# Optimization experiments

Hardware: AMD Instinct MI355X
Metric: run time of the kernel (lower is better)

Reference implementation:

```python
import jax, jax.numpy as jnp
import numpy as np

TEMP1 = 4.0  # local_temp1 default


def setup_inputs() -> dict:
    key = jax.random.key(0)
    k1, k2 = jax.random.split(key)
    query = jax.random.normal(k1, (256, 768, 96), dtype=jnp.float32)
    context = jax.random.normal(k2, (256, 768, 19, 19), dtype=jnp.float32)
    return {"query": query, "context": context}


def reference(query, context):
    # query: [B, ndf, Q]; context: [B, ndf, ih, iw]
    B, ndf, Q = query.shape
    ih, iw = context.shape[2], context.shape[3]
    S = ih * iw
    ctx = context.reshape(B, ndf, S)            # [B, ndf, S]
    # attn = contextT @ query -> [B, S, Q]
    attn = jnp.einsum('bds,bdq->bsq', ctx, query)
    # softmax over query dim
    attn = jax.nn.softmax(attn, axis=-1)
    # transpose to [B, Q, S], temperature scale, softmax over source dim
    attn = jnp.swapaxes(attn, 1, 2) * TEMP1
    attn = jax.nn.softmax(attn, axis=-1)        # [B, Q, S]
    # weightedContext = context @ attn^T -> [B, ndf, Q]
    weighted_context = jnp.einsum('bds,bqs->bdq', ctx, attn)
    attn_map = attn.reshape(B, Q, ih, iw)
    return weighted_context, attn_map
```

## Files before the change

### kernel.cpp

```cpp
#include <hip/hip_runtime.h>

#define NB 256
#define NDF 768
#define NQ 96
#define NS 361
#define LDT 40
#define LDP 392
#define WSROW 368
#define WS_LOG_BYTES ((size_t)NB * NQ * WSROW * 2)

typedef short bf16x8_t __attribute__((ext_vector_type(8)));
typedef float f32x2_t __attribute__((ext_vector_type(2)));
typedef float f32x4_t __attribute__((ext_vector_type(4)));
typedef float f32x4u_t __attribute__((ext_vector_type(4), aligned(4)));
typedef unsigned int u32x4_t __attribute__((ext_vector_type(4)));

__device__ __forceinline__ unsigned pack_hi(unsigned b_, unsigned a_) {
    return __builtin_amdgcn_perm(b_, a_, 0x07060302u);
}
__device__ __forceinline__ unsigned short f2bf(float x) {
    unsigned u = __float_as_uint(x);
    u += 0x7FFFu + ((u >> 16) & 1u);
    return (unsigned short)(u >> 16);
}
__device__ __forceinline__ float bf2f(unsigned short h) {
    return __uint_as_float(((unsigned)h) << 16);
}

__device__ __forceinline__ void cvt8(const float* x, bf16x8_t& hi, bf16x8_t& lo) {
    unsigned uh[8]; float fl[8];
#pragma unroll
    for (int j = 0; j < 8; ++j) {
        unsigned u = __float_as_uint(x[j]);
        uh[j] = u;
        fl[j] = x[j] - __uint_as_float(u & 0xFFFF0000u);
    }
    u32x4_t h, l;
    h[0] = pack_hi(uh[1], uh[0]); h[1] = pack_hi(uh[3], uh[2]);
    h[2] = pack_hi(uh[5], uh[4]); h[3] = pack_hi(uh[7], uh[6]);
    l[0] = pack_hi(__float_as_uint(fl[1]), __float_as_uint(fl[0]));
    l[1] = pack_hi(__float_as_uint(fl[3]), __float_as_uint(fl[2]));
    l[2] = pack_hi(__float_as_uint(fl[5]), __float_as_uint(fl[4]));
    l[3] = pack_hi(__float_as_uint(fl[7]), __float_as_uint(fl[6]));
    hi = __builtin_bit_cast(bf16x8_t, h);
    lo = __builtin_bit_cast(bf16x8_t, l);
}

__device__ __forceinline__ void block_sync_lds() {
    asm volatile("s_waitcnt lgkmcnt(0)" ::: "memory");
    __builtin_amdgcn_s_barrier();
    __builtin_amdgcn_sched_barrier(0);
}

#define GLD(D, A)       asm volatile("global_load_dword %0, %1, off" : "=v"(D) : "v"(A))
#define GLDO(D, A, O)   asm volatile("global_load_dword %0, %1, off offset:" #O : "=v"(D) : "v"(A))
#define GLD2(D, A)      asm volatile("global_load_dwordx2 %0, %1, off" : "=v"(D) : "v"(A))
#define GLD2O(D, A, O)  asm volatile("global_load_dwordx2 %0, %1, off offset:" #O : "=v"(D) : "v"(A))
#define VMWAIT(N) { asm volatile("s_waitcnt vmcnt(" #N ")"); __builtin_amdgcn_sched_barrier(0); }

template<int MODE>
__global__ __launch_bounds__(384, 3) void k1_gemm1_softmaxq(
    const float* __restrict__ Qg, const float* __restrict__ Cg,
    unsigned short* __restrict__ WsLog, float* __restrict__ AoutF)
{
    __shared__ __align__(16) unsigned short sQhi[2][NQ * LDT];
    __shared__ __align__(16) unsigned short sQlo[2][NQ * LDT];

    const int x = blockIdx.x;
    const int b = (x & 7) * 32 + (x >> 4);
    const int h = (x >> 3) & 1;

    const int tid = threadIdx.x;
    const int wv = tid >> 6;
    const int lane = tid & 63;
    const int ll = lane & 15;
    const int lg = lane >> 4;
    const int llh = (ll >> 3) & 1;
    const int s0 = 192 * h;
    const int qq = tid % 96;
    const int koct = tid / 96;
    const int spRaw = s0 + 32 * wv + 2 * ll;
    const int sp0c  = min(spRaw, NS - 2);
    const bool bsel = (spRaw > NS - 2);
    const int stoff = qq * LDT + 8 * (koct ^ ((qq >> 3) & 3));

    const float* __restrict__ qg = Qg + (size_t)b * NDF * NQ;
    const float* __restrict__ cg = Cg + (size_t)b * NDF * NS;
    const float* __restrict__ cgl = cg + sp0c;

    f32x4_t acc[6][2];
#pragma unroll
    for (int i = 0; i < 6; ++i)
#pragma unroll
        for (int j = 0; j < 2; ++j) acc[i][j] = (f32x4_t)0.0f;

    float qv0[8], qv1[8];
    f32x2_t rcA[8], rcB[8], rcC[8];

#define ISSUE_Q(K0, QV) { \
    unsigned long long qa = (unsigned long long)(qg + ((K0) + 8 * koct) * NQ + qq); \
    GLD (QV[0], qa);        GLDO(QV[1], qa, 384); \
    GLDO(QV[2], qa, 768);   GLDO(QV[3], qa, 1152); \
    GLDO(QV[4], qa, 1536);  GLDO(QV[5], qa, 1920); \
    GLDO(QV[6], qa, 2304);  GLDO(QV[7], qa, 2688); }

#define ISSUE_CTX(K0, R) { \
    unsigned long long p0 = (unsigned long long)(cgl + (size_t)((K0) + 8 * lg) * NS); \
    unsigned long long p1 = p0 + 3u * 1444u; \
    unsigned long long p2 = p0 + 6u * 1444u; \
    GLD2 (R[0], p0); GLD2O(R[1], p0, 1444); GLD2O(R[2], p0, 2888); \
    GLD2 (R[3], p1); GLD2O(R[4], p1, 1444); GLD2O(R[5], p1, 2888); \
    GLD2 (R[6], p2); GLD2O(R[7], p2, 1444); }

#define STAGEQ(QV, CUR) { \
    bf16x8_t qh, ql; \
    cvt8(QV, qh, ql); \
    *(bf16x8_t*)&sQhi[CUR][stoff] = qh; \
    *(bf16x8_t*)&sQlo[CUR][stoff] = ql; }

#define MFMAPH(R, CUR) { \
    float xe[8], xo[8]; \
    _Pragma("unroll") \
    for (int j = 0; j < 8; ++j) { \
        xe[j] = bsel ? R[j][1] : R[j][0]; \
        xo[j] = R[j][1]; } \
    bf16x8_t B0h, B0l, B1h, B1l; \
    cvt8(xe, B0h, B0l); \
    cvt8(xo, B1h, B1l); \
    _Pragma("unroll") \
    for (int mt = 0; mt < 6; ++mt) { \
        int ro = (16 * mt + ll) * LDT + 8 * (lg ^ ((2 * mt + llh) & 3)); \
        bf16x8_t Ah = *(const bf16x8_t*)&sQhi[CUR][ro]; \
        bf16x8_t Al = *(const bf16x8_t*)&sQlo[CUR][ro]; \
        acc[mt][0] = __builtin_amdgcn_mfma_f32_16x16x32_bf16(Ah, B0h, acc[mt][0], 0, 0, 0); \
        acc[mt][0] = __builtin_amdgcn_mfma_f32_16x16x32_bf16(Ah, B0l, acc[mt][0], 0, 0, 0); \
        acc[mt][0] = __builtin_amdgcn_mfma_f32_16x16x32_bf16(Al, B0h, acc[mt][0], 0, 0, 0); \
        acc[mt][1] = __builtin_amdgcn_mfma_f32_16x16x32_bf16(Ah, B1h, acc[mt][1], 0, 0, 0); \
        acc[mt][1] = __builtin_amdgcn_mfma_f32_16x16x32_bf16(Ah, B1l, acc[mt][1], 0, 0, 0); \
        acc[mt][1] = __builtin_amdgcn_mfma_f32_16x16x32_bf16(Al, B1h, acc[mt][1], 0, 0, 0); } }

#define ITER(C, USE, FILL, QISS, QSTG, CUR, NXT) { \
    ISSUE_Q(((C) + 2) * 32, QISS); \
    ISSUE_CTX(((C) + 2) * 32, FILL); \
    VMWAIT(32); \
    MFMAPH(USE, CUR); \
    VMWAIT(24); \
    STAGEQ(QSTG, NXT); \
    block_sync_lds(); }

    ISSUE_Q(0, qv0);   ISSUE_CTX(0, rcA);
    ISSUE_Q(32, qv1);  ISSUE_CTX(32, rcB);
    VMWAIT(24);
    STAGEQ(qv0, 0);
    block_sync_lds();

    for (int cc = 0; cc < 18; cc += 6) {
        ITER(cc + 0, rcA, rcC, qv0, qv1, 0, 1);
        ITER(cc + 1, rcB, rcA, qv1, qv0, 1, 0);
        ITER(cc + 2, rcC, rcB, qv0, qv1, 0, 1);
        ITER(cc + 3, rcA, rcC, qv1, qv0, 1, 0);
        ITER(cc + 4, rcB, rcA, qv0, qv1, 0, 1);
        ITER(cc + 5, rcC, rcB, qv1, qv0, 1, 0);
    }
    ITER(18, rcA, rcC, qv0, qv1, 0, 1);
    ITER(19, rcB, rcA, qv1, qv0, 1, 0);
    ITER(20, rcC, rcB, qv0, qv1, 0, 1);
    ITER(21, rcA, rcC, qv1, qv0, 1, 0);
    VMWAIT(16);
    MFMAPH(rcB, 0);
    VMWAIT(8);
    STAGEQ(qv1, 1);
    block_sync_lds();
    VMWAIT(0);
    MFMAPH(rcC, 1);

#undef ISSUE_Q
#undef ISSUE_CTX
#undef STAGEQ
#undef MFMAPH
#undef ITER

#pragma unroll
    for (int nt = 0; nt < 2; ++nt) {
        float m = -3.0e38f;
#pragma unroll
        for (int mt = 0; mt < 6; ++mt)
#pragma unroll
            for (int r = 0; r < 4; ++r) m = fmaxf(m, acc[mt][nt][r]);
        m = fmaxf(m, __shfl_xor(m, 16));
        m = fmaxf(m, __shfl_xor(m, 32));
        float sum = 0.0f;
#pragma unroll
        for (int mt = 0; mt < 6; ++mt)
#pragma unroll
            for (int r = 0; r < 4; ++r) {
                float e = __expf(acc[mt][nt][r] - m);
                acc[mt][nt][r] = e;
                sum += e;
            }
        sum += __shfl_xor(sum, 16);
        sum += __shfl_xor(sum, 32);
        float inv = 4.0f / sum;
#pragma unroll
        for (int mt = 0; mt < 6; ++mt)
#pragma unroll
            for (int r = 0; r < 4; ++r) acc[mt][nt][r] *= inv;
    }

    if constexpr (MODE >= 1) {
        unsigned short* wr = WsLog + (size_t)b * NQ * WSROW;
#pragma unroll
        for (int mt = 0; mt < 6; ++mt)
#pragma unroll
            for (int nt = 0; nt < 2; ++nt)
#pragma unroll
                for (int r = 0; r < 4; ++r) {
                    int q = 16 * mt + 4 * lg + r;
                    int s = s0 + 32 * wv + 2 * ll + nt;
                    if (s < NS) wr[q * WSROW + s] = f2bf(acc[mt][nt][r]);
                }
    } else {
        float* aout = AoutF + (size_t)b * NQ * NS;
#pragma unroll
        for (int mt = 0; mt < 6; ++mt)
#pragma unroll
            for (int nt = 0; nt < 2; ++nt)
#pragma unroll
                for (int r = 0; r < 4; ++r) {
                    int q = 16 * mt + 4 * lg + r;
                    int s = s0 + 32 * wv + 2 * ll + nt;
                    if (s < NS) aout[(size_t)q * NS + s] = acc[mt][nt][r];
                }
    }
}

__global__ __launch_bounds__(256) void k15_softmaxs(float* __restrict__ Aout)
{
    const int b = blockIdx.x;
    const int q = blockIdx.y * 4 + (threadIdx.x >> 6);
    const int lane = threadIdx.x & 63;
    float* __restrict__ row = Aout + ((size_t)b * NQ + q) * NS;
    const int c0 = 6 * lane;

    float v[6];
#pragma unroll
    for (int i = 0; i < 6; ++i) v[i] = (c0 + i < NS) ? row[c0 + i] : -INFINITY;
    float m = v[0];
#pragma unroll
    for (int i = 1; i < 6; ++i) m = fmaxf(m, v[i]);
#pragma unroll
    for (int o = 1; o < 64; o <<= 1) m = fmaxf(m, __shfl_xor(m, o));
    float e[6], sum = 0.0f;
#pragma unroll
    for (int i = 0; i < 6; ++i) { e[i] = __expf(v[i] - m); sum += e[i]; }
#pragma unroll
    for (int o = 1; o < 64; o <<= 1) sum += __shfl_xor(sum, o);
    float inv = 1.0f / sum;
#pragma unroll
    for (int i = 0; i < 6; ++i) if (c0 + i < NS) row[c0 + i] = e[i] * inv;
}

template<bool FUSED>
__global__ __launch_bounds__(512, 4) void k2_gemm2(
    const float* __restrict__ Cg, const unsigned short* __restrict__ WsLog,
    const float* __restrict__ AttnF, float* __restrict__ Wout, float* __restrict__ AoutF)
{
    extern __shared__ char smem2[];
    unsigned short* sP = (unsigned short*)smem2;
    unsigned* sPd = (unsigned*)smem2;
    float* sMax = (float*)(smem2 + NQ * LDP * 2);
    float* sInv = sMax + NQ;

    const int x = blockIdx.x;
    const int b = (x & 7) * 32 + (x >> 5);
    const int quarter = (x >> 3) & 3;
    const int tid = threadIdx.x;
    const int wv = tid >> 6;
    const int lane = tid & 63;
    const int ll = lane & 15;
    const int lg = lane >> 4;

    if constexpr (FUSED) {
        const unsigned* __restrict__ wsd = (const unsigned*)(WsLog + (size_t)b * NQ * WSROW);
        for (int i = tid; i < NQ * 184; i += 512) {
            int r = i / 184, c = i - r * 184;
            sPd[r * 196 + c] = wsd[i];
        }
        for (int i = tid; i < NQ * 12; i += 512) {
            int r = i / 12, c = i - r * 12;
            sPd[r * 196 + 184 + c] = 0;
        }
        __syncthreads();

        const int l32 = tid & 31;
        const int rbase = tid >> 5;
#pragma unroll
        for (int pass = 0; pass < 6; ++pass) {
            int row = pass * 16 + rbase;
            float m = -3.0e38f;
#pragma unroll
            for (int j = 0; j < 6; ++j) {
                int dw = l32 + 32 * j;
                if (dw < 184) {
                    unsigned u = sPd[row * 196 + dw];
                    float v0 = bf2f((unsigned short)(u & 0xFFFFu));
                    float v1 = bf2f((unsigned short)(u >> 16));
                    if (2 * dw < NS) m = fmaxf(m, v0);
                    if (2 * dw + 1 < NS) m = fmaxf(m, v1);
                }
            }
#pragma unroll
            for (int o = 1; o < 32; o <<= 1) m = fmaxf(m, __shfl_xor(m, o));
            if (l32 == 0) sMax[row] = m;
        }
        __syncthreads();
#pragma unroll
        for (int pass = 0; pass < 6; ++pass) {
            int row = pass * 16 + rbase;
            float m = sMax[row];
            float sum = 0.0f;
#pragma unroll
            for (int j = 0; j < 6; ++j) {
                int dw = l32 + 32 * j;
                if (dw < 184) {
                    unsigned u = sPd[row * 196 + dw];
                    float v0 = bf2f((unsigned short)(u & 0xFFFFu));
                    float v1 = bf2f((unsigned short)(u >> 16));
                    float e0 = (2 * dw < NS) ? __expf(v0 - m) : 0.0f;
                    float e1 = (2 * dw + 1 < NS) ? __expf(v1 - m) : 0.0f;
                    sum += e0 + e1;
                    sPd[row * 196 + dw] = ((unsigned)f2bf(e1) << 16) | (unsigned)f2bf(e0);
                }
            }
#pragma unroll
            for (int o = 1; o < 32; o <<= 1) sum += __shfl_xor(sum, o);
            if (l32 == 0) sInv[row] = sum;
        }
        __syncthreads();
        if (tid < NQ) sInv[tid] = 1.0f / sInv[tid];
        __syncthreads();
        if (quarter == 0) {
            float* aout = AoutF + (size_t)b * NQ * NS;
            for (int i = tid; i < NQ * NS; i += 512) {
                int q = i / NS, s = i - q * NS;
                aout[i] = bf2f(sP[q * LDP + s]) * sInv[q];
            }
        }
    } else {
        const float* __restrict__ attn = AttnF + (size_t)b * NQ * NS;
        for (int i = tid; i < NQ * 181; i += 512) {
            int row = i / 181, p = i - row * 181;
            float x0 = attn[row * NS + 2 * p];
            float x1 = (p < 180) ? attn[row * NS + 2 * p + 1] : 0.0f;
            sPd[row * 196 + p] = pack_hi(__float_as_uint(x1), __float_as_uint(x0));
        }
        for (int i = tid; i < NQ * 15; i += 512) {
            int row = i / 15, p = i - row * 15;
            sPd[row * 196 + 181 + p] = 0;
        }
        __syncthreads();
    }

    f32x4_t acc[3][3];
#pragma unroll
    for (int i = 0; i < 3; ++i)
#pragma unroll
        for (int j = 0; j < 3; ++j) acc[i][j] = (f32x4_t)0.0f;

    const int dw = wv >> 1, qw = wv & 1;
    const float* __restrict__ cq = Cg + (size_t)b * NDF * NS + (size_t)(quarter * 192) * NS;

#pragma unroll
    for (int c = 0; c < 12; ++c) {
        bf16x8_t Bf[3];
#pragma unroll
        for (int nt = 0; nt < 3; ++nt) {
            int row = 16 * (3 * qw + nt) + ll;
            Bf[nt] = *(const bf16x8_t*)&sP[row * LDP + 32 * c + 8 * lg];
        }
#pragma unroll
        for (int i = 0; i < 3; ++i) {
            int d = 16 * (3 * dw + i) + ll;
            const float* ap = cq + (size_t)d * NS + 32 * c + 8 * lg;
            u32x4_t u;
            if (c < 11) {
                f32x4u_t a0 = *(const f32x4u_t*)ap;
                f32x4u_t a1 = *(const f32x4u_t*)(ap + 4);
                u[0] = pack_hi(__float_as_uint(a0[1]), __float_as_uint(a0[0]));
                u[1] = pack_hi(__float_as_uint(a0[3]), __float_as_uint(a0[2]));
                u[2] = pack_hi(__float_as_uint(a1[1]), __float_as_uint(a1[0]));
                u[3] = pack_hi(__float_as_uint(a1[3]), __float_as_uint(a1[2]));
            } else {
                float t[8];
#pragma unroll
                for (int e = 0; e < 8; ++e) {
                    int s = 352 + 8 * lg + e;
                    t[e] = (s < NS) ? ap[e] : 0.0f;
                }
                u[0] = pack_hi(__float_as_uint(t[1]), __float_as_uint(t[0]));
                u[1] = pack_hi(__float_as_uint(t[3]), __float_as_uint(t[2]));
                u[2] = pack_hi(__float_as_uint(t[5]), __float_as_uint(t[4]));
                u[3] = pack_hi(__float_as_uint(t[7]), __float_as_uint(t[6]));
            }
            bf16x8_t Af = __builtin_bit_cast(bf16x8_t, u);
#pragma unroll
            for (int nt = 0; nt < 3; ++nt)
                acc[i][nt] = __builtin_amdgcn_mfma_f32_16x16x32_bf16(Af, Bf[nt], acc[i][nt], 0, 0, 0);
        }
    }

    float* wout = Wout + (size_t)b * NDF * NQ;
    float invq[3];
#pragma unroll
    for (int nt = 0; nt < 3; ++nt) {
        if constexpr (FUSED) invq[nt] = sInv[16 * (3 * qw + nt) + ll];
        else invq[nt] = 1.0f;
    }
#pragma unroll
    for (int i = 0; i < 3; ++i)
#pragma unroll
        for (int nt = 0; nt < 3; ++nt)
#pragma unroll
            for (int r = 0; r < 4; ++r) {
                int d = quarter * 192 + 16 * (3 * dw + i) + 4 * lg + r;
                int q = 16 * (3 * qw + nt) + ll;
                wout[(size_t)d * NQ + q] = acc[i][nt][r] * invq[nt];
            }
}

extern "C" void kernel_launch(void* const* d_in, const int* in_sizes, int n_in,
                              void* d_out, int out_size, void* d_ws, size_t ws_size,
                              hipStream_t stream) {
    const float* Qg = (const float*)d_in[0];
    const float* Cg = (const float*)d_in[1];
    float* Wout = (float*)d_out;
    float* Aout = Wout + (size_t)NB * NDF * NQ;

    const int smem2 = NQ * LDP * 2 + NQ * 8;

    if (ws_size >= WS_LOG_BYTES) {
        unsigned short* wsLog = (unsigned short*)d_ws;
        k1_gemm1_softmaxq<1><<<dim3(NB * 2), dim3(384), 0, stream>>>(Qg, Cg, wsLog, nullptr);
        (void)hipFuncSetAttribute((const void*)k2_gemm2<true>,
                                  hipFuncAttributeMaxDynamicSharedMemorySize, smem2);
        k2_gemm2<true><<<dim3(NB * 4), dim3(512), smem2, stream>>>(
            Cg, wsLog, nullptr, Wout, Aout);
    } else {
        k1_gemm1_softmaxq<0><<<dim3(NB * 2), dim3(384), 0, stream>>>(Qg, Cg, nullptr, Aout);
        k15_softmaxs<<<dim3(NB, 24), dim3(256), 0, stream>>>(Aout);
        (void)hipFuncSetAttribute((const void*)k2_gemm2<false>,
                                  hipFuncAttributeMaxDynamicSharedMemorySize, smem2);
        k2_gemm2<false><<<dim3(NB * 4), dim3(512), smem2, stream>>>(
            Cg, nullptr, Aout, Wout, Aout);
    }
}
```

Baseline: 212.0 us.

## Emit bf16 context copy from gemm1 and read it in gemm2

The first kernel now writes a bf16-truncated, padded copy of the context tensor to workspace while it streams the context for GEMM1. The second kernel reads those bf16 rows directly instead of reloading fp32 context and packing it, which roughly halves GEMM2's context traffic. The GEMM1 pipeline also moves from triple to double buffering of context registers with adjusted wait counts, which lowers register pressure. The cost is extra global stores in kernel 1 and a larger workspace requirement, with the old paths kept as fallbacks when the workspace is too small.

```diff
diff --git a/kernel.cpp b/kernel.cpp
--- a/kernel.cpp
+++ b/kernel.cpp
@@ -7,7 +7,10 @@
 #define LDT 40
 #define LDP 392
 #define WSROW 368
+#define CSROW 368
 #define WS_LOG_BYTES ((size_t)NB * NQ * WSROW * 2)
+#define WS_CTX_BYTES ((size_t)NB * NDF * CSROW * 2)
+#define WS_FULL_BYTES (WS_LOG_BYTES + WS_CTX_BYTES)
 
 typedef short bf16x8_t __attribute__((ext_vector_type(8)));
 typedef float f32x2_t __attribute__((ext_vector_type(2)));
@@ -56,12 +59,16 @@
 #define GLDO(D, A, O)   asm volatile("global_load_dword %0, %1, off offset:" #O : "=v"(D) : "v"(A))
 #define GLD2(D, A)      asm volatile("global_load_dwordx2 %0, %1, off" : "=v"(D) : "v"(A))
 #define GLD2O(D, A, O)  asm volatile("global_load_dwordx2 %0, %1, off offset:" #O : "=v"(D) : "v"(A))
-#define VMWAIT(N) { asm volatile("s_waitcnt vmcnt(" #N ")"); __builtin_amdgcn_sched_barrier(0); }
+#define GST(A, D)       asm volatile("global_store_dword %0, %1, off" :: "v"(A), "v"(D))
+#define GSTO(A, D, O)   asm volatile("global_store_dword %0, %1, off offset:" #O :: "v"(A), "v"(D))
+#define VMWAIT_(N) { asm volatile("s_waitcnt vmcnt(" #N ")"); __builtin_amdgcn_sched_barrier(0); }
+#define VMWAIT(N) VMWAIT_(N)
 
 template<int MODE>
 __global__ __launch_bounds__(384, 3) void k1_gemm1_softmaxq(
     const float* __restrict__ Qg, const float* __restrict__ Cg,
-    unsigned short* __restrict__ WsLog, float* __restrict__ AoutF)
+    unsigned short* __restrict__ WsLog, unsigned* __restrict__ WsCtxD,
+    float* __restrict__ AoutF)
 {
     __shared__ __align__(16) unsigned short sQhi[2][NQ * LDT];
     __shared__ __align__(16) unsigned short sQlo[2][NQ * LDT];
@@ -82,11 +89,14 @@
     const int spRaw = s0 + 32 * wv + 2 * ll;
     const int sp0c  = min(spRaw, NS - 2);
     const bool bsel = (spRaw > NS - 2);
+    const int pairIdx = 96 * h + 16 * wv + ll;
+    const bool wok = (MODE == 2) && (pairIdx <= 180);
     const int stoff = qq * LDT + 8 * (koct ^ ((qq >> 3) & 3));
 
     const float* __restrict__ qg = Qg + (size_t)b * NDF * NQ;
     const float* __restrict__ cg = Cg + (size_t)b * NDF * NS;
     const float* __restrict__ cgl = cg + sp0c;
+    unsigned* __restrict__ wsc = (MODE == 2) ? (WsCtxD + (size_t)b * NDF * 184 + pairIdx) : nullptr;
 
     f32x4_t acc[6][2];
 #pragma unroll
@@ -94,15 +104,15 @@
 #pragma unroll
         for (int j = 0; j < 2; ++j) acc[i][j] = (f32x4_t)0.0f;
 
-    float qv0[8], qv1[8];
-    f32x2_t rcA[8], rcB[8], rcC[8];
-
-#define ISSUE_Q(K0, QV) { \
+    float qv[8];
+    f32x2_t rcA[8], rcB[8];
+
+#define ISSUE_Q(K0) { \
     unsigned long long qa = (unsigned long long)(qg + ((K0) + 8 * koct) * NQ + qq); \
-    GLD (QV[0], qa);        GLDO(QV[1], qa, 384); \
-    GLDO(QV[2], qa, 768);   GLDO(QV[3], qa, 1152); \
-    GLDO(QV[4], qa, 1536);  GLDO(QV[5], qa, 1920); \
-    GLDO(QV[6], qa, 2304);  GLDO(QV[7], qa, 2688); }
+    GLD (qv[0], qa);        GLDO(qv[1], qa, 384); \
+    GLDO(qv[2], qa, 768);   GLDO(qv[3], qa, 1152); \
+    GLDO(qv[4], qa, 1536);  GLDO(qv[5], qa, 1920); \
+    GLDO(qv[6], qa, 2304);  GLDO(qv[7], qa, 2688); }
 
 #define ISSUE_CTX(K0, R) { \
     unsigned long long p0 = (unsigned long long)(cgl + (size_t)((K0) + 8 * lg) * NS); \
@@ -112,9 +122,24 @@
     GLD2 (R[3], p1); GLD2O(R[4], p1, 1444); GLD2O(R[5], p1, 2888); \
     GLD2 (R[6], p2); GLD2O(R[7], p2, 1444); }
 
-#define STAGEQ(QV, CUR) { \
+#define ISSUE_ST(K0, R) { \
+    if (wok) { \
+        unsigned st[8]; \
+        _Pragma("unroll") \
+        for (int j = 0; j < 8; ++j) { \
+            unsigned lo_ = bsel ? __float_as_uint(R[j][1]) : __float_as_uint(R[j][0]); \
+            unsigned hi_ = bsel ? 0u : __float_as_uint(R[j][1]); \
+            st[j] = pack_hi(hi_, lo_); \
+        } \
+        unsigned long long a0 = (unsigned long long)(wsc + (size_t)((K0) + 8 * lg) * 184); \
+        unsigned long long a1 = a0 + 4416u; \
+        GST (a0, st[0]); GSTO(a0, st[1], 736); GSTO(a0, st[2], 1472); \
+        GSTO(a0, st[3], 2208); GSTO(a0, st[4], 2944); GSTO(a0, st[5], 3680); \
+        GST (a1, st[6]); GSTO(a1, st[7], 736); } }
+
+#define STAGEQ(CUR) { \
     bf16x8_t qh, ql; \
-    cvt8(QV, qh, ql); \
+    cvt8(qv, qh, ql); \
     *(bf16x8_t*)&sQhi[CUR][stoff] = qh; \
     *(bf16x8_t*)&sQlo[CUR][stoff] = ql; }
 
@@ -139,43 +164,44 @@
         acc[mt][1] = __builtin_amdgcn_mfma_f32_16x16x32_bf16(Ah, B1l, acc[mt][1], 0, 0, 0); \
         acc[mt][1] = __builtin_amdgcn_mfma_f32_16x16x32_bf16(Al, B1h, acc[mt][1], 0, 0, 0); } }
 
-#define ITER(C, USE, FILL, QISS, QSTG, CUR, NXT) { \
-    ISSUE_Q(((C) + 2) * 32, QISS); \
-    ISSUE_CTX(((C) + 2) * 32, FILL); \
-    VMWAIT(32); \
+#define ITER(C, USE, FILL, CUR, NXT, W1, W2) { \
+    ISSUE_Q(((C) + 1) * 32); \
+    ISSUE_CTX(((C) + 1) * 32, FILL); \
+    VMWAIT(W1); \
+    ISSUE_ST((C) * 32, USE); \
     MFMAPH(USE, CUR); \
-    VMWAIT(24); \
-    STAGEQ(QSTG, NXT); \
+    VMWAIT(W2); \
+    STAGEQ(NXT); \
     block_sync_lds(); }
 
-    ISSUE_Q(0, qv0);   ISSUE_CTX(0, rcA);
-    ISSUE_Q(32, qv1);  ISSUE_CTX(32, rcB);
-    VMWAIT(24);
-    STAGEQ(qv0, 0);
+    ISSUE_Q(0);
+    ISSUE_CTX(0, rcA);
+    VMWAIT(8);
+    STAGEQ(0);
     block_sync_lds();
 
-    for (int cc = 0; cc < 18; cc += 6) {
-        ITER(cc + 0, rcA, rcC, qv0, qv1, 0, 1);
-        ITER(cc + 1, rcB, rcA, qv1, qv0, 1, 0);
-        ITER(cc + 2, rcC, rcB, qv0, qv1, 0, 1);
-        ITER(cc + 3, rcA, rcC, qv1, qv0, 1, 0);
-        ITER(cc + 4, rcB, rcA, qv0, qv1, 0, 1);
-        ITER(cc + 5, rcC, rcB, qv1, qv0, 1, 0);
-    }
-    ITER(18, rcA, rcC, qv0, qv1, 0, 1);
-    ITER(19, rcB, rcA, qv1, qv0, 1, 0);
-    ITER(20, rcC, rcB, qv0, qv1, 0, 1);
-    ITER(21, rcA, rcC, qv1, qv0, 1, 0);
-    VMWAIT(16);
-    MFMAPH(rcB, 0);
-    VMWAIT(8);
-    STAGEQ(qv1, 1);
-    block_sync_lds();
-    VMWAIT(0);
-    MFMAPH(rcC, 1);
+    if constexpr (MODE == 2) {
+        ITER(0, rcA, rcB, 0, 1, 16, 16);
+        for (int c = 1; c < 22; c += 2) {
+            ITER(c,     rcB, rcA, 1, 0, 24, 16);
+            ITER(c + 1, rcA, rcB, 0, 1, 24, 16);
+        }
+        VMWAIT(8);
+        ISSUE_ST(23 * 32, rcB);
+        MFMAPH(rcB, 1);
+    } else {
+        ITER(0, rcA, rcB, 0, 1, 16, 8);
+        for (int c = 1; c < 22; c += 2) {
+            ITER(c,     rcB, rcA, 1, 0, 16, 8);
+            ITER(c + 1, rcA, rcB, 0, 1, 16, 8);
+        }
+        VMWAIT(0);
+        MFMAPH(rcB, 1);
+    }
 
 #undef ISSUE_Q
 #undef ISSUE_CTX
+#undef ISSUE_ST
 #undef STAGEQ
 #undef MFMAPH
 #undef ITER
@@ -232,6 +258,7 @@
                     if (s < NS) aout[(size_t)q * NS + s] = acc[mt][nt][r];
                 }
     }
+    asm volatile("s_waitcnt vmcnt(0)" ::: "memory");
 }
 
 __global__ __launch_bounds__(256) void k15_softmaxs(float* __restrict__ Aout)
@@ -260,9 +287,10 @@
     for (int i = 0; i < 6; ++i) if (c0 + i < NS) row[c0 + i] = e[i] * inv;
 }
 
-template<bool FUSED>
+template<int MODE>
 __global__ __launch_bounds__(512, 4) void k2_gemm2(
     const float* __restrict__ Cg, const unsigned short* __restrict__ WsLog,
+    const unsigned short* __restrict__ WsCtx,
     const float* __restrict__ AttnF, float* __restrict__ Wout, float* __restrict__ AoutF)
 {
     extern __shared__ char smem2[];
@@ -280,7 +308,7 @@
     const int ll = lane & 15;
     const int lg = lane >> 4;
 
-    if constexpr (FUSED) {
+    if constexpr (MODE >= 1) {
         const unsigned* __restrict__ wsd = (const unsigned*)(WsLog + (size_t)b * NQ * WSROW);
         for (int i = tid; i < NQ * 184; i += 512) {
             int r = i / 184, c = i - r * 184;
@@ -369,6 +397,8 @@
 
     const int dw = wv >> 1, qw = wv & 1;
     const float* __restrict__ cq = Cg + (size_t)b * NDF * NS + (size_t)(quarter * 192) * NS;
+    const unsigned short* __restrict__ cb =
+        (MODE == 2) ? (WsCtx + ((size_t)b * NDF + quarter * 192) * CSROW) : nullptr;
 
 #pragma unroll
     for (int c = 0; c < 12; ++c) {
@@ -381,28 +411,37 @@
 #pragma unroll
         for (int i = 0; i < 3; ++i) {
             int d = 16 * (3 * dw + i) + ll;
-            const float* ap = cq + (size_t)d * NS + 32 * c + 8 * lg;
-            u32x4_t u;
-            if (c < 11) {
-                f32x4u_t a0 = *(const f32x4u_t*)ap;
-                f32x4u_t a1 = *(const f32x4u_t*)(ap + 4);
-                u[0] = pack_hi(__float_as_uint(a0[1]), __float_as_uint(a0[0]));
-                u[1] = pack_hi(__float_as_uint(a0[3]), __float_as_uint(a0[2]));
-                u[2] = pack_hi(__float_as_uint(a1[1]), __float_as_uint(a1[0]));
-                u[3] = pack_hi(__float_as_uint(a1[3]), __float_as_uint(a1[2]));
+            bf16x8_t Af;
+            if constexpr (MODE == 2) {
+                if (c < 11 || lg < 2) {
+                    Af = *(const bf16x8_t*)&cb[(size_t)d * CSROW + 32 * c + 8 * lg];
+                } else {
+                    Af = (bf16x8_t)0;
+                }
             } else {
-                float t[8];
-#pragma unroll
-                for (int e = 0; e < 8; ++e) {
-                    int s = 352 + 8 * lg + e;
-                    t[e] = (s < NS) ? ap[e] : 0.0f;
+                const float* ap = cq + (size_t)d * NS + 32 * c + 8 * lg;
+                u32x4_t u;
+                if (c < 11) {
+                    f32x4u_t a0 = *(const f32x4u_t*)ap;
+                    f32x4u_t a1 = *(const f32x4u_t*)(ap + 4);
+                    u[0] = pack_hi(__float_as_uint(a0[1]), __float_as_uint(a0[0]));
+                    u[1] = pack_hi(__float_as_uint(a0[3]), __float_as_uint(a0[2]));
+                    u[2] = pack_hi(__float_as_uint(a1[1]), __float_as_uint(a1[0]));
+                    u[3] = pack_hi(__float_as_uint(a1[3]), __float_as_uint(a1[2]));
+                } else {
+                    float t[8];
+#pragma unroll
+                    for (int e = 0; e < 8; ++e) {
+                        int s = 352 + 8 * lg + e;
+                        t[e] = (s < NS) ? ap[e] : 0.0f;
+                    }
+                    u[0] = pack_hi(__float_as_uint(t[1]), __float_as_uint(t[0]));
+                    u[1] = pack_hi(__float_as_uint(t[3]), __float_as_uint(t[2]));
+                    u[2] = pack_hi(__float_as_uint(t[5]), __float_as_uint(t[4]));
+                    u[3] = pack_hi(__float_as_uint(t[7]), __float_as_uint(t[6]));
                 }
-                u[0] = pack_hi(__float_as_uint(t[1]), __float_as_uint(t[0]));
-                u[1] = pack_hi(__float_as_uint(t[3]), __float_as_uint(t[2]));
-                u[2] = pack_hi(__float_as_uint(t[5]), __float_as_uint(t[4]));
-                u[3] = pack_hi(__float_as_uint(t[7]), __float_as_uint(t[6]));
+                Af = __builtin_bit_cast(bf16x8_t, u);
             }
-            bf16x8_t Af = __builtin_bit_cast(bf16x8_t, u);
 #pragma unroll
             for (int nt = 0; nt < 3; ++nt)
                 acc[i][nt] = __builtin_amdgcn_mfma_f32_16x16x32_bf16(Af, Bf[nt], acc[i][nt], 0, 0, 0);
@@ -413,7 +452,7 @@
     float invq[3];
 #pragma unroll
     for (int nt = 0; nt < 3; ++nt) {
-        if constexpr (FUSED) invq[nt] = sInv[16 * (3 * qw + nt) + ll];
+        if constexpr (MODE >= 1) invq[nt] = sInv[16 * (3 * qw + nt) + ll];
         else invq[nt] = 1.0f;
     }
 #pragma unroll
@@ -438,19 +477,27 @@
 
     const int smem2 = NQ * LDP * 2 + NQ * 8;
 
-    if (ws_size >= WS_LOG_BYTES) {
+    if (ws_size >= WS_FULL_BYTES) {
         unsigned short* wsLog = (unsigned short*)d_ws;
-        k1_gemm1_softmaxq<1><<<dim3(NB * 2), dim3(384), 0, stream>>>(Qg, Cg, wsLog, nullptr);
-        (void)hipFuncSetAttribute((const void*)k2_gemm2<true>,
+        unsigned* wsCtxD = (unsigned*)((char*)d_ws + WS_LOG_BYTES);
+        k1_gemm1_softmaxq<2><<<dim3(NB * 2), dim3(384), 0, stream>>>(Qg, Cg, wsLog, wsCtxD, nullptr);
+        (void)hipFuncSetAttribute((const void*)k2_gemm2<2>,
                                   hipFuncAttributeMaxDynamicSharedMemorySize, smem2);
-        k2_gemm2<true><<<dim3(NB * 4), dim3(512), smem2, stream>>>(
-            Cg, wsLog, nullptr, Wout, Aout);
+        k2_gemm2<2><<<dim3(NB * 4), dim3(512), smem2, stream>>>(
+            Cg, wsLog, (const unsigned short*)wsCtxD, nullptr, Wout, Aout);
+    } else if (ws_size >= WS_LOG_BYTES) {
+        unsigned short* wsLog = (unsigned short*)d_ws;
+        k1_gemm1_softmaxq<1><<<dim3(NB * 2), dim3(384), 0, stream>>>(Qg, Cg, wsLog, nullptr, nullptr);
+        (void)hipFuncSetAttribute((const void*)k2_gemm2<1>,
+                                  hipFuncAttributeMaxDynamicSharedMemorySize, smem2);
+        k2_gemm2<1><<<dim3(NB * 4), dim3(512), smem2, stream>>>(
+            Cg, wsLog, nullptr, nullptr, Wout, Aout);
     } else {
-        k1_gemm1_softmaxq<0><<<dim3(NB * 2), dim3(384), 0, stream>>>(Qg, Cg, nullptr, Aout);
+        k1_gemm1_softmaxq<0><<<dim3(NB * 2), dim3(384), 0, stream>>>(Qg, Cg, nullptr, nullptr, Aout);
         k15_softmaxs<<<dim3(NB, 24), dim3(256), 0, stream>>>(Aout);
-        (void)hipFuncSetAttribute((const void*)k2_gemm2<false>,
+        (void)hipFuncSetAttribute((const void*)k2_gemm2<0>,
                                   hipFuncAttributeMaxDynamicSharedMemorySize, smem2);
-        k2_gemm2<false><<<dim3(NB * 4), dim3(512), smem2, stream>>>(
-            Cg, nullptr, Aout, Wout, Aout);
-    }
-}
+        k2_gemm2<0><<<dim3(NB * 4), dim3(512), smem2, stream>>>(
+            Cg, nullptr, nullptr, Aout, Wout, Aout);
+    }
+}
```

Result: no change. 211.9 us (-0.1%).

## Load query operand directly into registers, dropping LDS staging and barriers

Applied to the files above, without the earlier changes.

The first GEMM kernel no longer stages the query tile through shared memory with double buffering and block barriers. Each lane now loads its own 48 query values straight from global memory into registers and splits them into bf16 hi/lo pairs right before the MFMAs. The context prefetch pipeline shrinks from triple to double buffering. This removes LDS traffic and workgroup syncs, but each wave now redundantly fetches and converts the full query tile, which raises global and L2 load traffic, conversion ALU work and register pressure, and the prefetch depth is lower.

```diff
diff --git a/kernel.cpp b/kernel.cpp
--- a/kernel.cpp
+++ b/kernel.cpp
@@ -4,7 +4,6 @@
 #define NDF 768
 #define NQ 96
 #define NS 361
-#define LDT 40
 #define LDP 392
 #define WSROW 368
 #define WS_LOG_BYTES ((size_t)NB * NQ * WSROW * 2)
@@ -46,26 +45,18 @@
     lo = __builtin_bit_cast(bf16x8_t, l);
 }
 
-__device__ __forceinline__ void block_sync_lds() {
-    asm volatile("s_waitcnt lgkmcnt(0)" ::: "memory");
-    __builtin_amdgcn_s_barrier();
-    __builtin_amdgcn_sched_barrier(0);
-}
-
 #define GLD(D, A)       asm volatile("global_load_dword %0, %1, off" : "=v"(D) : "v"(A))
 #define GLDO(D, A, O)   asm volatile("global_load_dword %0, %1, off offset:" #O : "=v"(D) : "v"(A))
 #define GLD2(D, A)      asm volatile("global_load_dwordx2 %0, %1, off" : "=v"(D) : "v"(A))
 #define GLD2O(D, A, O)  asm volatile("global_load_dwordx2 %0, %1, off offset:" #O : "=v"(D) : "v"(A))
-#define VMWAIT(N) { asm volatile("s_waitcnt vmcnt(" #N ")"); __builtin_amdgcn_sched_barrier(0); }
+#define VMWAIT_(N) { asm volatile("s_waitcnt vmcnt(" #N ")"); __builtin_amdgcn_sched_barrier(0); }
+#define VMWAIT(N) VMWAIT_(N)
 
 template<int MODE>
 __global__ __launch_bounds__(384, 3) void k1_gemm1_softmaxq(
     const float* __restrict__ Qg, const float* __restrict__ Cg,
     unsigned short* __restrict__ WsLog, float* __restrict__ AoutF)
 {
-    __shared__ __align__(16) unsigned short sQhi[2][NQ * LDT];
-    __shared__ __align__(16) unsigned short sQlo[2][NQ * LDT];
-
     const int x = blockIdx.x;
     const int b = (x & 7) * 32 + (x >> 4);
     const int h = (x >> 3) & 1;
@@ -75,18 +66,13 @@
     const int lane = tid & 63;
     const int ll = lane & 15;
     const int lg = lane >> 4;
-    const int llh = (ll >> 3) & 1;
     const int s0 = 192 * h;
-    const int qq = tid % 96;
-    const int koct = tid / 96;
     const int spRaw = s0 + 32 * wv + 2 * ll;
     const int sp0c  = min(spRaw, NS - 2);
     const bool bsel = (spRaw > NS - 2);
-    const int stoff = qq * LDT + 8 * (koct ^ ((qq >> 3) & 3));
-
-    const float* __restrict__ qg = Qg + (size_t)b * NDF * NQ;
-    const float* __restrict__ cg = Cg + (size_t)b * NDF * NS;
-    const float* __restrict__ cgl = cg + sp0c;
+
+    const float* __restrict__ qg  = Qg + (size_t)b * NDF * NQ;
+    const float* __restrict__ cgl = Cg + (size_t)b * NDF * NS + sp0c;
 
     f32x4_t acc[6][2];
 #pragma unroll
@@ -94,31 +80,29 @@
 #pragma unroll
         for (int j = 0; j < 2; ++j) acc[i][j] = (f32x4_t)0.0f;
 
-    float qv0[8], qv1[8];
-    f32x2_t rcA[8], rcB[8], rcC[8];
-
-#define ISSUE_Q(K0, QV) { \
-    unsigned long long qa = (unsigned long long)(qg + ((K0) + 8 * koct) * NQ + qq); \
-    GLD (QV[0], qa);        GLDO(QV[1], qa, 384); \
-    GLDO(QV[2], qa, 768);   GLDO(QV[3], qa, 1152); \
-    GLDO(QV[4], qa, 1536);  GLDO(QV[5], qa, 1920); \
-    GLDO(QV[6], qa, 2304);  GLDO(QV[7], qa, 2688); }
-
-#define ISSUE_CTX(K0, R) { \
-    unsigned long long p0 = (unsigned long long)(cgl + (size_t)((K0) + 8 * lg) * NS); \
+    float qv[48];
+    f32x2_t rcA[8], rcB[8];
+
+#define QLD(MT) { \
+    unsigned long long a_ = qa + (MT) * 64ull; \
+    GLD (qv[(MT)*8+0], a_);        GLDO(qv[(MT)*8+1], a_, 384); \
+    GLDO(qv[(MT)*8+2], a_, 768);   GLDO(qv[(MT)*8+3], a_, 1152); \
+    GLDO(qv[(MT)*8+4], a_, 1536);  GLDO(qv[(MT)*8+5], a_, 1920); \
+    GLDO(qv[(MT)*8+6], a_, 2304);  GLDO(qv[(MT)*8+7], a_, 2688); }
+
+#define ISSUE_Q(C) { \
+    unsigned long long qa = (unsigned long long)(qg + ((C) * 32 + 8 * lg) * NQ + ll); \
+    QLD(0); QLD(1); QLD(2); QLD(3); QLD(4); QLD(5); }
+
+#define ISSUE_CTX(C, R) { \
+    unsigned long long p0 = (unsigned long long)(cgl + (size_t)((C) * 32 + 8 * lg) * NS); \
     unsigned long long p1 = p0 + 3u * 1444u; \
     unsigned long long p2 = p0 + 6u * 1444u; \
     GLD2 (R[0], p0); GLD2O(R[1], p0, 1444); GLD2O(R[2], p0, 2888); \
     GLD2 (R[3], p1); GLD2O(R[4], p1, 1444); GLD2O(R[5], p1, 2888); \
     GLD2 (R[6], p2); GLD2O(R[7], p2, 1444); }
 
-#define STAGEQ(QV, CUR) { \
-    bf16x8_t qh, ql; \
-    cvt8(QV, qh, ql); \
-    *(bf16x8_t*)&sQhi[CUR][stoff] = qh; \
-    *(bf16x8_t*)&sQlo[CUR][stoff] = ql; }
-
-#define MFMAPH(R, CUR) { \
+#define CVTMFMA(R) { \
     float xe[8], xo[8]; \
     _Pragma("unroll") \
     for (int j = 0; j < 8; ++j) { \
@@ -129,9 +113,8 @@
     cvt8(xo, B1h, B1l); \
     _Pragma("unroll") \
     for (int mt = 0; mt < 6; ++mt) { \
-        int ro = (16 * mt + ll) * LDT + 8 * (lg ^ ((2 * mt + llh) & 3)); \
-        bf16x8_t Ah = *(const bf16x8_t*)&sQhi[CUR][ro]; \
-        bf16x8_t Al = *(const bf16x8_t*)&sQlo[CUR][ro]; \
+        bf16x8_t Ah, Al; \
+        cvt8(&qv[mt * 8], Ah, Al); \
         acc[mt][0] = __builtin_amdgcn_mfma_f32_16x16x32_bf16(Ah, B0h, acc[mt][0], 0, 0, 0); \
         acc[mt][0] = __builtin_amdgcn_mfma_f32_16x16x32_bf16(Ah, B0l, acc[mt][0], 0, 0, 0); \
         acc[mt][0] = __builtin_amdgcn_mfma_f32_16x16x32_bf16(Al, B0h, acc[mt][0], 0, 0, 0); \
@@ -139,46 +122,31 @@
         acc[mt][1] = __builtin_amdgcn_mfma_f32_16x16x32_bf16(Ah, B1l, acc[mt][1], 0, 0, 0); \
         acc[mt][1] = __builtin_amdgcn_mfma_f32_16x16x32_bf16(Al, B1h, acc[mt][1], 0, 0, 0); } }
 
-#define ITER(C, USE, FILL, QISS, QSTG, CUR, NXT) { \
-    ISSUE_Q(((C) + 2) * 32, QISS); \
-    ISSUE_CTX(((C) + 2) * 32, FILL); \
-    VMWAIT(32); \
-    MFMAPH(USE, CUR); \
-    VMWAIT(24); \
-    STAGEQ(QSTG, NXT); \
-    block_sync_lds(); }
-
-    ISSUE_Q(0, qv0);   ISSUE_CTX(0, rcA);
-    ISSUE_Q(32, qv1);  ISSUE_CTX(32, rcB);
-    VMWAIT(24);
-    STAGEQ(qv0, 0);
-    block_sync_lds();
-
-    for (int cc = 0; cc < 18; cc += 6) {
-        ITER(cc + 0, rcA, rcC, qv0, qv1, 0, 1);
-        ITER(cc + 1, rcB, rcA, qv1, qv0, 1, 0);
-        ITER(cc + 2, rcC, rcB, qv0, qv1, 0, 1);
-        ITER(cc + 3, rcA, rcC, qv1, qv0, 1, 0);
-        ITER(cc + 4, rcB, rcA, qv0, qv1, 0, 1);
-        ITER(cc + 5, rcC, rcB, qv1, qv0, 1, 0);
-    }
-    ITER(18, rcA, rcC, qv0, qv1, 0, 1);
-    ITER(19, rcB, rcA, qv1, qv0, 1, 0);
-    ITER(20, rcC, rcB, qv0, qv1, 0, 1);
-    ITER(21, rcA, rcC, qv1, qv0, 1, 0);
-    VMWAIT(16);
-    MFMAPH(rcB, 0);
-    VMWAIT(8);
-    STAGEQ(qv1, 1);
-    block_sync_lds();
-    VMWAIT(0);
-    MFMAPH(rcC, 1);
-
+#define BODYF(C, USE, FILL) { \
+    ISSUE_Q(C); \
+    ISSUE_CTX((C) + 1, FILL); \
+    VMWAIT(8); \
+    CVTMFMA(USE); }
+
+#define BODYL(C, USE) { \
+    ISSUE_Q(C); \
+    VMWAIT(0); \
+    CVTMFMA(USE); }
+
+    ISSUE_CTX(0, rcA);
+    for (int c = 0; c < 22; c += 2) {
+        BODYF(c,     rcA, rcB);
+        BODYF(c + 1, rcB, rcA);
+    }
+    BODYF(22, rcA, rcB);
+    BODYL(23, rcB);
+
+#undef QLD
 #undef ISSUE_Q
 #undef ISSUE_CTX
-#undef STAGEQ
-#undef MFMAPH
-#undef ITER
+#undef CVTMFMA
+#undef BODYF
+#undef BODYL
 
 #pragma unroll
     for (int nt = 0; nt < 2; ++nt) {
```

Result: slower. 255.9 us (+20.7%).
